# Optimization experiments

Measured on AMD Instinct MI355X. Metric: run time of the kernel, lower is better.

## Reference

```python
import jax, jax.numpy as jnp
import numpy as np

EPS = 1e-5

def conv2d(x, w, stride, pad):
    return jax.lax.conv_general_dilated(
        x, w, window_strides=(stride, stride),
        padding=[(pad, pad), (pad, pad)],
        dimension_numbers=('NCHW', 'OIHW', 'NCHW'))

def batchnorm(x, gamma, beta, mean, var):
    # inference-mode BN over channel dim of NCHW
    inv = jax.lax.rsqrt(var + EPS)
    return (x - mean[None, :, None, None]) * (inv * gamma)[None, :, None, None] + beta[None, :, None, None]

def rational(x, num, den):
    # Rational activation, version A, degrees (5,4):
    #   P(x) = num0 + num1*x + ... + num5*x^5  (Horner)
    #   Q(x) = 1 + sum_{j=1..4} |den_{j-1}| * |x|^j
    p = num[5]
    for i in range(4, -1, -1):
        p = p * x + num[i]
    xa = jnp.abs(x)
    q = jnp.ones_like(x)
    pw = xa
    for j in range(4):
        q = q + jnp.abs(den[j]) * pw
        pw = pw * xa
    return p / q

def multi_variant_rationals(out, num_r, den_r, num_g, den_g, num_b, den_b):
    # channels 0::3 -> r, 1::3 -> g, 2::3 -> b, then re-interleave
    B, C, H, W = out.shape
    o = out.reshape(B, C // 3, 3, H, W)  # channel c = 3*j + k
    r = rational(o[:, :, 0], num_r, den_r)
    g = rational(o[:, :, 1], num_g, den_g)
    b = rational(o[:, :, 2], num_b, den_b)
    return jnp.stack([r, g, b], axis=2).reshape(B, C, H, W)

def setup_inputs() -> dict:
    key = jax.random.key(0)
    ks = jax.random.split(key, 12)
    B, Cin, Cout, H, W = 64, 96, 192, 56, 56
    inp = {
        'x': jax.random.normal(ks[0], (B, Cin, H, W), jnp.float32),
        'w1': jax.random.normal(ks[1], (Cout, Cin, 3, 3), jnp.float32) * 0.05,
        'gamma1': jnp.ones((Cout,), jnp.float32),
        'beta1': jnp.zeros((Cout,), jnp.float32),
        'mean1': jnp.zeros((Cout,), jnp.float32),
        'var1': jnp.ones((Cout,), jnp.float32),
        'num_r': jax.random.normal(ks[2], (6,), jnp.float32) * 0.3,
        'den_r': jax.random.normal(ks[3], (4,), jnp.float32) * 0.3,
        'num_g': jax.random.normal(ks[4], (6,), jnp.float32) * 0.3,
        'den_g': jax.random.normal(ks[5], (4,), jnp.float32) * 0.3,
        'num_b': jax.random.normal(ks[6], (6,), jnp.float32) * 0.3,
        'den_b': jax.random.normal(ks[7], (4,), jnp.float32) * 0.3,
        'w2': jax.random.normal(ks[8], (Cout, Cout, 3, 3), jnp.float32) * 0.05,
        'gamma2': jnp.ones((Cout,), jnp.float32),
        'beta2': jnp.zeros((Cout,), jnp.float32),
        'mean2': jnp.zeros((Cout,), jnp.float32),
        'var2': jnp.ones((Cout,), jnp.float32),
        'ws': jax.random.normal(ks[9], (Cout, Cin, 1, 1), jnp.float32) * 0.05,
        'gammas': jnp.ones((Cout,), jnp.float32),
        'betas': jnp.zeros((Cout,), jnp.float32),
        'means': jnp.zeros((Cout,), jnp.float32),
        'vars_': jnp.ones((Cout,), jnp.float32),
    }
    return inp

def reference(x, w1, gamma1, beta1, mean1, var1,
              num_r, den_r, num_g, den_g, num_b, den_b,
              w2, gamma2, beta2, mean2, var2,
              ws, gammas, betas, means, vars_):
    STRIDE = 2
    out = batchnorm(conv2d(x, w1, STRIDE, 1), gamma1, beta1, mean1, var1)
    out = multi_variant_rationals(out, num_r, den_r, num_g, den_g, num_b, den_b)
    out = batchnorm(conv2d(out, w2, 1, 1), gamma2, beta2, mean2, var2)
    shortcut = batchnorm(conv2d(x, ws, STRIDE, 0), gammas, betas, means, vars_)
    out = out + shortcut
    out = multi_variant_rationals(out, num_r, den_r, num_g, den_g, num_b, den_b)
    return out
```

## Files before the change

kernel.cpp:

```cpp
#include <hip/hip_runtime.h>

#define EPSBN  1e-5f
#define NBLK   392

#define W1B_OFF 0u
#define W2B_OFF 331776u
#define WSB_OFF 995328u
#define CS_OFF  1044480u
#define XT_OFF  1048320u
#define ACT_OFF 39583488u

typedef __attribute__((ext_vector_type(8))) short bf16x8;
typedef __attribute__((ext_vector_type(4))) short bf16x4;
typedef __attribute__((ext_vector_type(4))) float f32x4;

__device__ __forceinline__ short f2bf(float f) {
    unsigned u = __float_as_uint(f);
    u += 0x7fffu + ((u >> 16) & 1u);
    return (short)(u >> 16);
}

__device__ __forceinline__ void gload16(const short* g, short* l) {
    __builtin_amdgcn_global_load_lds(
        (const __attribute__((address_space(1))) void*)g,
        (__attribute__((address_space(3))) void*)l, 16, 0, 0);
}

__device__ __forceinline__ float rational_eval(float v, const float* nm, const float* dn) {
    float p = nm[5];
    p = p * v + nm[4];
    p = p * v + nm[3];
    p = p * v + nm[2];
    p = p * v + nm[1];
    p = p * v + nm[0];
    float xa = fabsf(v);
    float q = 1.0f;
    float pw = xa;
    q += dn[0] * pw; pw *= xa;
    q += dn[1] * pw; pw *= xa;
    q += dn[2] * pw; pw *= xa;
    q += dn[3] * pw;
    float inv = __builtin_amdgcn_rcpf(q);
    inv = inv * (2.0f - q * inv);
    return p * inv;
}

__device__ __forceinline__ void sel_coeffs(int v, const float cnm[3][6], const float cdn[3][4],
                                           float nm[6], float dn[4]) {
#pragma unroll
    for (int i = 0; i < 6; i++) nm[i] = (v == 0) ? cnm[0][i] : ((v == 1) ? cnm[1][i] : cnm[2][i]);
#pragma unroll
    for (int i = 0; i < 4; i++) dn[i] = (v == 0) ? cdn[0][i] : ((v == 1) ? cdn[1][i] : cdn[2][i]);
}

extern "C" __global__ void prep_scales_kernel(
    const float* g1, const float* b1, const float* m1, const float* v1,
    const float* g2, const float* b2, const float* m2, const float* v2,
    const float* gs, const float* bs, const float* ms, const float* vs,
    float* cs)
{
    int i = threadIdx.x;
    if (i < 192) {
        float a1 = g1[i] * rsqrtf(v1[i] + EPSBN);
        float a2 = g2[i] * rsqrtf(v2[i] + EPSBN);
        float a3 = gs[i] * rsqrtf(vs[i] + EPSBN);
        cs[i]       = a1;
        cs[192 + i] = a2;
        cs[384 + i] = a3;
        cs[576 + i] = b1[i] - m1[i] * a1;
        cs[768 + i] = (b2[i] - m2[i] * a2) + (bs[i] - ms[i] * a3);
    }
}

extern "C" __global__ void prep_w_kernel(const float* __restrict__ w, const float* __restrict__ s,
                                         short* __restrict__ wb, int CI_src, int CI_dst, int KP, int total)
{
    int i = blockIdx.x * 256 + threadIdx.x;
    if (i >= total) return;
    int co = i / (CI_dst * KP);
    int r  = i - co * CI_dst * KP;
    int kpos = r / CI_dst;
    int ci = r - kpos * CI_dst;
    wb[i] = (ci < CI_src) ? f2bf(w[(co * CI_src + ci) * KP + kpos] * s[co]) : (short)0;
}

extern "C" __global__ void ring_zero_kernel(short* __restrict__ buf, int H, int C, int total)
{
    int ring = 2 * H + 2 * (H - 2);
    int i = blockIdx.x * 256 + threadIdx.x;
    if (i >= total) return;
    int c = i % C;
    int t = i / C;
    int rp = t % ring;
    int n = t / ring;
    int h, w;
    if (rp < H)           { h = 0;          w = rp; }
    else if (rp < 2 * H)  { h = H - 1;      w = rp - H; }
    else { int k = rp - 2 * H; h = (k >> 1) + 1; w = (k & 1) ? (H - 1) : 0; }
    buf[((n * H + h) * H + w) * C + c] = 0;
}

extern "C" __global__ __launch_bounds__(256)
void xpose_kernel(const float* __restrict__ x, short* __restrict__ xt)
{
    __shared__ float t[96 * 57];
    int b = blockIdx.x;
    int n = b / 56, h = b - n * 56;
    const float* src = x + n * (96 * 3136) + h * 56;
    for (int i = threadIdx.x; i < 96 * 28; i += 256) {
        int c = i / 28, w2 = i - c * 28;
        float2 v = *(const float2*)&src[c * 3136 + w2 * 2];
        t[c * 57 + w2 * 2]     = v.x;
        t[c * 57 + w2 * 2 + 1] = v.y;
    }
    __syncthreads();
    unsigned* dst = (unsigned*)(xt + (n * 56 + h) * 56 * 96);
    for (int i = threadIdx.x; i < 56 * 48; i += 256) {
        int w = i / 96 * 0 + i / 48, cp = i - (i / 48) * 48;
        unsigned lo = (unsigned short)f2bf(t[(2 * cp) * 57 + w]);
        unsigned hi = (unsigned short)f2bf(t[(2 * cp + 1) * 57 + w]);
        dst[w * 48 + cp] = lo | (hi << 16);
    }
}

extern "C" __global__ __launch_bounds__(512, 4)
void convA_kernel(const short* __restrict__ xt,
                  const short* __restrict__ w1b,
                  const short* __restrict__ zbuf,
                  const float* __restrict__ bias1,
                  const float* __restrict__ num_r, const float* __restrict__ den_r,
                  const float* __restrict__ num_g, const float* __restrict__ den_g,
                  const float* __restrict__ num_b, const float* __restrict__ den_b,
                  short* __restrict__ act)
{
    __shared__ short lA[2][192 * 32];
    __shared__ short lB[2][128 * 32];

    const int tid  = threadIdx.x;
    const int lane = tid & 63;
    const int wave = tid >> 6;
    const int wm = wave >> 1, wn = wave & 1;
    const int lbid = (blockIdx.x & 7) * 49 + (blockIdx.x >> 3);
    const int p0   = lbid * 128;

    const int sA = (((tid & 3) ^ ((tid >> 3) & 3))) * 8;
    const int r1 = tid >> 2;
    const int aw1a = r1 * 864 + sA;
    const int aw1b = (128 + r1) * 864 + sA;

    int xb0; bool top, left;
    {
        int p = p0 + r1;
        int n = p / 784; int pr = p - n * 784;
        int oh = pr / 28; int ow = pr - oh * 28;
        xb0 = ((n * 56 + 2 * oh) * 56 + 2 * ow) * 96 + sA;
        top = (oh == 0); left = (ow == 0);
    }

    const int l15 = lane & 15, ksl = lane >> 4;
    int ard[3], brd[4];
#pragma unroll
    for (int m = 0; m < 3; ++m) {
        int row = wm * 48 + m * 16 + l15;
        ard[m] = row * 32 + ((ksl ^ ((row >> 1) & 3)) << 3);
    }
#pragma unroll
    for (int n = 0; n < 4; ++n) {
        int row = wn * 64 + n * 16 + l15;
        brd[n] = row * 32 + ((ksl ^ ((row >> 1) & 3)) << 3);
    }

    auto stage = [&](int buf, int t) {
        int kpos = t / 3, cb = t - 3 * kpos;
        int kh = kpos / 3, kw = kpos - 3 * kh;
        gload16(&w1b[aw1a + t * 32], &lA[buf][wave * 512]);
        if (tid < 256) gload16(&w1b[aw1b + t * 32], &lA[buf][4096 + wave * 512]);
        int bko = ((kh - 1) * 56 + (kw - 1)) * 96 + cb * 32;
        const short* src = (((kh == 0) && top) || ((kw == 0) && left)) ? zbuf : &xt[xb0 + bko];
        gload16(src, &lB[buf][wave * 512]);
    };

    f32x4 acc[3][4];
#pragma unroll
    for (int m = 0; m < 3; m++)
#pragma unroll
        for (int n = 0; n < 4; n++) acc[m][n] = (f32x4){0.f, 0.f, 0.f, 0.f};

    stage(0, 0);
    int cur = 0;
    for (int t = 0; t < 27; ++t) {
        __syncthreads();
        if (t + 1 < 27) stage(cur ^ 1, t + 1);
        bf16x8 af[3];
#pragma unroll
        for (int m = 0; m < 3; ++m) af[m] = *(const bf16x8*)&lA[cur][ard[m]];
#pragma unroll
        for (int n = 0; n < 4; ++n) {
            bf16x8 bv = *(const bf16x8*)&lB[cur][brd[n]];
#pragma unroll
            for (int m = 0; m < 3; ++m)
                acc[m][n] = __builtin_amdgcn_mfma_f32_16x16x32_bf16(af[m], bv, acc[m][n], 0, 0, 0);
        }
        cur ^= 1;
    }

    float cnm[3][6], cdn[3][4];
#pragma unroll
    for (int i = 0; i < 6; i++) { cnm[0][i] = num_r[i]; cnm[1][i] = num_g[i]; cnm[2][i] = num_b[i]; }
#pragma unroll
    for (int i = 0; i < 4; i++) { cdn[0][i] = fabsf(den_r[i]); cdn[1][i] = fabsf(den_g[i]); cdn[2][i] = fabsf(den_b[i]); }

    int abase[4];
#pragma unroll
    for (int n = 0; n < 4; ++n) {
        int pp = p0 + wn * 64 + n * 16 + l15;
        int n2 = pp / 784; int r2 = pp - n2 * 784;
        int oh2 = r2 / 28; int ow2 = r2 - oh2 * 28;
        abase[n] = ((n2 * 30 + oh2 + 1) * 30 + ow2 + 1) * 192;
    }
#pragma unroll
    for (int m = 0; m < 3; ++m) {
        int cob = wm * 48 + m * 16 + (ksl << 2);
        float res[4][4];
#pragma unroll
        for (int r = 0; r < 4; ++r) {
            float nm[6], dn[4];
            sel_coeffs((cob + r) % 3, cnm, cdn, nm, dn);
            float bv = bias1[cob + r];
#pragma unroll
            for (int n = 0; n < 4; ++n)
                res[n][r] = rational_eval(acc[m][n][r] + bv, nm, dn);
        }
#pragma unroll
        for (int n = 0; n < 4; ++n) {
            bf16x4 pk;
#pragma unroll
            for (int r = 0; r < 4; ++r) pk[r] = f2bf(res[n][r]);
            *(bf16x4*)&act[abase[n] + cob] = pk;
        }
    }
}

extern "C" __global__ __launch_bounds__(512, 4)
void convB_kernel(const short* __restrict__ act,
                  const short* __restrict__ xt,
                  const short* __restrict__ w2b,
                  const short* __restrict__ wsb,
                  const float* __restrict__ bias2s,
                  const float* __restrict__ num_r, const float* __restrict__ den_r,
                  const float* __restrict__ num_g, const float* __restrict__ den_g,
                  const float* __restrict__ num_b, const float* __restrict__ den_b,
                  float* __restrict__ outp)
{
    __shared__ short lA[2][192 * 64];
    __shared__ short lB[2][128 * 64];

    const int tid  = threadIdx.x;
    const int lane = tid & 63;
    const int wave = tid >> 6;
    const int wm = wave >> 1, wn = wave & 1;
    const int lbid = (blockIdx.x & 7) * 49 + (blockIdx.x >> 3);
    const int p0   = lbid * 128;

    const int s8 = (((tid & 7) ^ ((tid >> 3) & 7))) * 8;
    const int rA = tid >> 3;

    int awW[3], awS[3];
#pragma unroll
    for (int c = 0; c < 3; ++c) {
        int row = c * 64 + rA;
        awW[c] = row * 1728 + s8;
        awS[c] = row * 128 + s8;
    }
    int abB[2], xcB[2];
#pragma unroll
    for (int c = 0; c < 2; ++c) {
        int p = p0 + c * 64 + rA;
        int n = p / 784; int pr = p - n * 784;
        int oh = pr / 28; int ow = pr - oh * 28;
        abB[c] = ((n * 30 + oh) * 30 + ow) * 192 + s8;
        xcB[c] = ((n * 56 + 2 * oh) * 56 + 2 * ow) * 96 + s8;
    }

    const int l15 = lane & 15, ksl = lane >> 4;
    int ard[2][3], brd[2][4];
#pragma unroll
    for (int kk = 0; kk < 2; ++kk) {
#pragma unroll
        for (int m = 0; m < 3; ++m) {
            int row = wm * 48 + m * 16 + l15;
            ard[kk][m] = row * 64 + ((((kk << 2) | ksl) ^ (row & 7)) << 3);
        }
#pragma unroll
        for (int n = 0; n < 4; ++n) {
            int row = wn * 64 + n * 16 + l15;
            brd[kk][n] = row * 64 + ((((kk << 2) | ksl) ^ (row & 7)) << 3);
        }
    }

    auto stage = [&](int buf, int t) {
        if (t < 2) {
#pragma unroll
            for (int c = 0; c < 3; ++c)
                gload16(&wsb[awS[c] + t * 64], &lA[buf][c * 4096 + wave * 512]);
#pragma unroll
            for (int c = 0; c < 2; ++c)
                gload16(&xt[xcB[c] + t * 64], &lB[buf][c * 4096 + wave * 512]);
        } else {
            int u = t - 2;
            int kpos = u / 3, cb = u - 3 * kpos;
            int kh = kpos / 3, kw = kpos - 3 * kh;
            int bko = (kh * 30 + kw) * 192 + cb * 64;
#pragma unroll
            for (int c = 0; c < 3; ++c)
                gload16(&w2b[awW[c] + u * 64], &lA[buf][c * 4096 + wave * 512]);
#pragma unroll
            for (int c = 0; c < 2; ++c)
                gload16(&act[abB[c] + bko], &lB[buf][c * 4096 + wave * 512]);
        }
    };

    f32x4 acc[3][4];
#pragma unroll
    for (int m = 0; m < 3; m++)
#pragma unroll
        for (int n = 0; n < 4; n++) acc[m][n] = (f32x4){0.f, 0.f, 0.f, 0.f};

    stage(0, 0);
    int cur = 0;
    for (int t = 0; t < 29; ++t) {
        __syncthreads();
        if (t + 1 < 29) stage(cur ^ 1, t + 1);
#pragma unroll
        for (int kk = 0; kk < 2; ++kk) {
            bf16x8 af[3];
#pragma unroll
            for (int m = 0; m < 3; ++m) af[m] = *(const bf16x8*)&lA[cur][ard[kk][m]];
#pragma unroll
            for (int n = 0; n < 4; ++n) {
                bf16x8 bv = *(const bf16x8*)&lB[cur][brd[kk][n]];
#pragma unroll
                for (int m = 0; m < 3; ++m)
                    acc[m][n] = __builtin_amdgcn_mfma_f32_16x16x32_bf16(af[m], bv, acc[m][n], 0, 0, 0);
            }
        }
        cur ^= 1;
    }

    float cnm[3][6], cdn[3][4];
#pragma unroll
    for (int i = 0; i < 6; i++) { cnm[0][i] = num_r[i]; cnm[1][i] = num_g[i]; cnm[2][i] = num_b[i]; }
#pragma unroll
    for (int i = 0; i < 4; i++) { cdn[0][i] = fabsf(den_r[i]); cdn[1][i] = fabsf(den_g[i]); cdn[2][i] = fabsf(den_b[i]); }

    int obase[4];
#pragma unroll
    for (int n = 0; n < 4; ++n) {
        int pp = p0 + wn * 64 + n * 16 + l15;
        int n2 = pp / 784; int r2 = pp - n2 * 784;
        int oh2 = r2 / 28; int ow2 = r2 - oh2 * 28;
        obase[n] = n2 * (192 * 784) + oh2 * 28 + ow2;
    }
#pragma unroll
    for (int m = 0; m < 3; ++m) {
        int cob = wm * 48 + m * 16 + (ksl << 2);
#pragma unroll
        for (int r = 0; r < 4; ++r) {
            float nm[6], dn[4];
            sel_coeffs((cob + r) % 3, cnm, cdn, nm, dn);
            float bv = bias2s[cob + r];
#pragma unroll
            for (int n = 0; n < 4; ++n) {
                int idx = obase[n] + (cob + r) * 784;
                outp[idx] = rational_eval(acc[m][n][r] + bv, nm, dn);
            }
        }
    }
}

extern "C" void kernel_launch(void* const* d_in, const int* in_sizes, int n_in,
                              void* d_out, int out_size, void* d_ws, size_t ws_size,
                              hipStream_t stream)
{
    const float* x      = (const float*)d_in[0];
    const float* w1     = (const float*)d_in[1];
    const float* gamma1 = (const float*)d_in[2];
    const float* beta1  = (const float*)d_in[3];
    const float* mean1  = (const float*)d_in[4];
    const float* var1   = (const float*)d_in[5];
    const float* num_r  = (const float*)d_in[6];
    const float* den_r  = (const float*)d_in[7];
    const float* num_g  = (const float*)d_in[8];
    const float* den_g  = (const float*)d_in[9];
    const float* num_b  = (const float*)d_in[10];
    const float* den_b  = (const float*)d_in[11];
    const float* w2     = (const float*)d_in[12];
    const float* gamma2 = (const float*)d_in[13];
    const float* beta2  = (const float*)d_in[14];
    const float* mean2  = (const float*)d_in[15];
    const float* var2   = (const float*)d_in[16];
    const float* wsc    = (const float*)d_in[17];
    const float* gammas = (const float*)d_in[18];
    const float* betas  = (const float*)d_in[19];
    const float* means  = (const float*)d_in[20];
    const float* vars_  = (const float*)d_in[21];

    char* base = (char*)d_ws;
    short* w1b  = (short*)(base + W1B_OFF);
    short* w2b  = (short*)(base + W2B_OFF);
    short* wsb  = (short*)(base + WSB_OFF);
    float* cs   = (float*)(base + CS_OFF);
    short* xt   = (short*)(base + XT_OFF);
    short* act  = (short*)(base + ACT_OFF);
    float* outp = (float*)d_out;

    float* bias1  = cs + 576;
    float* bias2s = cs + 768;
    const short* zbuf = wsb + 96;

    prep_scales_kernel<<<1, 256, 0, stream>>>(gamma1, beta1, mean1, var1,
                                              gamma2, beta2, mean2, var2,
                                              gammas, betas, means, vars_, cs);

    prep_w_kernel<<<(192 * 96 * 9 + 255) / 256, 256, 0, stream>>>(w1, cs, w1b, 96, 96, 9, 192 * 96 * 9);
    prep_w_kernel<<<(192 * 192 * 9 + 255) / 256, 256, 0, stream>>>(w2, cs + 192, w2b, 192, 192, 9, 192 * 192 * 9);
    prep_w_kernel<<<(192 * 128 + 255) / 256, 256, 0, stream>>>(wsc, cs + 384, wsb, 96, 128, 1, 192 * 128);

    {
        int tot_a = 64 * (2 * 30 + 2 * 28) * 192;
        ring_zero_kernel<<<(tot_a + 255) / 256, 256, 0, stream>>>(act, 30, 192, tot_a);
    }

    xpose_kernel<<<64 * 56, 256, 0, stream>>>(x, xt);

    convA_kernel<<<NBLK, 512, 0, stream>>>(xt, w1b, zbuf, bias1,
                                           num_r, den_r, num_g, den_g, num_b, den_b,
                                           act);

    convB_kernel<<<NBLK, 512, 0, stream>>>(act, xt, w2b, wsb, bias2s,
                                           num_r, den_r, num_g, den_g, num_b, den_b,
                                           outp);
}
```

Baseline: 143.8 us.

## Restructure convB to stage a shared activation patch in LDS and reuse it across taps

convB now assigns each block one image and a band of 7 output rows (196 pixels, 224 including padding). It loads the 9x30x192 activation patch into LDS once with an XOR swizzle, and the 3x3 taps read shifted windows of that patch instead of reloading im2col tiles from global memory for every K step. Only the w2 weights are double-buffered through LDS. The 1x1 shortcut reads its operands straight from global memory into registers. The aim is to cut redundant activation traffic across the 9 taps, at the cost of larger LDS use (occupancy hint drops to 2), padding waste in the N dimension (224 vs 196), and fewer blocks (256).

```diff
diff --git a/kernel.cpp b/kernel.cpp
--- a/kernel.cpp
+++ b/kernel.cpp
@@ -1,7 +1,8 @@
 #include <hip/hip_runtime.h>
 
 #define EPSBN  1e-5f
-#define NBLK   392
+#define NBLK_A 392
+#define NBLK_B 256
 
 #define W1B_OFF 0u
 #define W2B_OFF 331776u
@@ -116,7 +117,7 @@
     __syncthreads();
     unsigned* dst = (unsigned*)(xt + (n * 56 + h) * 56 * 96);
     for (int i = threadIdx.x; i < 56 * 48; i += 256) {
-        int w = i / 96 * 0 + i / 48, cp = i - (i / 48) * 48;
+        int w = i / 48, cp = i - (i / 48) * 48;
         unsigned lo = (unsigned short)f2bf(t[(2 * cp) * 57 + w]);
         unsigned hi = (unsigned short)f2bf(t[(2 * cp + 1) * 57 + w]);
         dst[w * 48 + cp] = lo | (hi << 16);
@@ -241,7 +242,7 @@
     }
 }
 
-extern "C" __global__ __launch_bounds__(512, 4)
+extern "C" __global__ __launch_bounds__(512, 2)
 void convB_kernel(const short* __restrict__ act,
                   const short* __restrict__ xt,
                   const short* __restrict__ w2b,
@@ -252,98 +253,116 @@
                   const float* __restrict__ num_b, const float* __restrict__ den_b,
                   float* __restrict__ outp)
 {
-    __shared__ short lA[2][192 * 64];
-    __shared__ short lB[2][128 * 64];
+    __shared__ short patch[53248];
+    __shared__ short lA[2][6144];
 
     const int tid  = threadIdx.x;
     const int lane = tid & 63;
     const int wave = tid >> 6;
     const int wm = wave >> 1, wn = wave & 1;
-    const int lbid = (blockIdx.x & 7) * 49 + (blockIdx.x >> 3);
-    const int p0   = lbid * 128;
-
-    const int s8 = (((tid & 7) ^ ((tid >> 3) & 7))) * 8;
-    const int rA = tid >> 3;
-
-    int awW[3], awS[3];
-#pragma unroll
-    for (int c = 0; c < 3; ++c) {
-        int row = c * 64 + rA;
-        awW[c] = row * 1728 + s8;
-        awS[c] = row * 128 + s8;
-    }
-    int abB[2], xcB[2];
-#pragma unroll
-    for (int c = 0; c < 2; ++c) {
-        int p = p0 + c * 64 + rA;
-        int n = p / 784; int pr = p - n * 784;
-        int oh = pr / 28; int ow = pr - oh * 28;
-        abB[c] = ((n * 30 + oh) * 30 + ow) * 192 + s8;
-        xcB[c] = ((n * 56 + 2 * oh) * 56 + 2 * ow) * 96 + s8;
-    }
+    const int img = blockIdx.x >> 2;
+    const int oh0 = (blockIdx.x & 3) * 7;
 
     const int l15 = lane & 15, ksl = lane >> 4;
-    int ard[2][3], brd[2][4];
-#pragma unroll
-    for (int kk = 0; kk < 2; ++kk) {
-#pragma unroll
-        for (int m = 0; m < 3; ++m) {
-            int row = wm * 48 + m * 16 + l15;
-            ard[kk][m] = row * 64 + ((((kk << 2) | ksl) ^ (row & 7)) << 3);
-        }
-#pragma unroll
-        for (int n = 0; n < 4; ++n) {
-            int row = wn * 64 + n * 16 + l15;
-            brd[kk][n] = row * 64 + ((((kk << 2) | ksl) ^ (row & 7)) << 3);
-        }
-    }
-
-    auto stage = [&](int buf, int t) {
-        if (t < 2) {
-#pragma unroll
-            for (int c = 0; c < 3; ++c)
-                gload16(&wsb[awS[c] + t * 64], &lA[buf][c * 4096 + wave * 512]);
-#pragma unroll
-            for (int c = 0; c < 2; ++c)
-                gload16(&xt[xcB[c] + t * 64], &lB[buf][c * 4096 + wave * 512]);
-        } else {
-            int u = t - 2;
-            int kpos = u / 3, cb = u - 3 * kpos;
-            int kh = kpos / 3, kw = kpos - 3 * kh;
-            int bko = (kh * 30 + kw) * 192 + cb * 64;
-#pragma unroll
-            for (int c = 0; c < 3; ++c)
-                gload16(&w2b[awW[c] + u * 64], &lA[buf][c * 4096 + wave * 512]);
-#pragma unroll
-            for (int c = 0; c < 2; ++c)
-                gload16(&act[abB[c] + bko], &lB[buf][c * 4096 + wave * 512]);
+
+    int F0[7], F1[7], F2[7], C7[7], SCB[7], OB[7];
+    bool VAL[7];
+#pragma unroll
+    for (int nf = 0; nf < 7; ++nf) {
+        int p = wn * 112 + nf * 16 + l15;
+        int orow = p / 28, ow = p - orow * 28;
+        int r0 = orow;            if (r0 > 8) r0 = 8;
+        int r1_ = orow + 1;       if (r1_ > 8) r1_ = 8;
+        int r2_ = orow + 2;       if (r2_ > 8) r2_ = 8;
+        F0[nf] = r0 * 5760 + ow * 192;
+        F1[nf] = r1_ * 5760 + ow * 192;
+        F2[nf] = r2_ * 5760 + ow * 192;
+        C7[nf] = ow & 7;
+        int ohc = oh0 + orow; if (ohc > 27) ohc = 27;
+        SCB[nf] = ((img * 56 + 2 * ohc) * 56 + 2 * ow) * 96 + ksl * 8;
+        OB[nf]  = img * (192 * 784) + (oh0 + orow) * 28 + ow;
+        VAL[nf] = (p < 196);
+    }
+    int ard[3], scA[3];
+#pragma unroll
+    for (int m = 0; m < 3; ++m) {
+        int row = wm * 48 + m * 16 + l15;
+        ard[m] = row * 32 + ((ksl ^ ((row >> 1) & 3)) << 3);
+        scA[m] = row * 128 + ksl * 8;
+    }
+
+    const int prow0 = (img * 30 + oh0) * 30;
+#pragma unroll
+    for (int j = 0; j < 13; ++j) {
+        int o = (j * 512 + tid) * 8;
+        if (o > 51832) o = 51832;
+        int r = o / 5760;
+        int rem = o - r * 5760;
+        int c = rem / 192;
+        int sl = (rem - c * 192) >> 3;
+        const short* src = &act[(prow0 + r * 30 + c) * 192 + ((sl ^ (c & 7)) << 3)];
+        gload16(src, &patch[(j * 512 + wave * 64) * 8]);
+    }
+
+    f32x4 acc[3][7];
+#pragma unroll
+    for (int m = 0; m < 3; m++)
+#pragma unroll
+        for (int nf = 0; nf < 7; nf++) acc[m][nf] = (f32x4){0.f, 0.f, 0.f, 0.f};
+
+#pragma unroll
+    for (int s = 0; s < 3; ++s) {
+        bf16x8 af[3], bfv[7];
+#pragma unroll
+        for (int m = 0; m < 3; ++m) af[m] = *(const bf16x8*)&wsb[scA[m] + s * 32];
+#pragma unroll
+        for (int nf = 0; nf < 7; ++nf) bfv[nf] = *(const bf16x8*)&xt[SCB[nf] + s * 32];
+#pragma unroll
+        for (int m = 0; m < 3; ++m)
+#pragma unroll
+            for (int nf = 0; nf < 7; ++nf)
+                acc[m][nf] = __builtin_amdgcn_mfma_f32_16x16x32_bf16(af[m], bfv[nf], acc[m][nf], 0, 0, 0);
+    }
+
+    auto stageA = [&](int buf, int u) {
+        int kpos = u / 6, cbk = u - 6 * kpos;
+        int base = kpos * 192 + cbk * 32;
+        {
+            int row = tid >> 2, slot = tid & 3;
+            gload16(&w2b[row * 1728 + base + ((slot ^ ((row >> 1) & 3)) << 3)],
+                    &lA[buf][wave * 512]);
+        }
+        if (tid < 256) {
+            int row = 128 + (tid >> 2), slot = tid & 3;
+            gload16(&w2b[row * 1728 + base + ((slot ^ ((row >> 1) & 3)) << 3)],
+                    &lA[buf][4096 + wave * 512]);
         }
     };
 
-    f32x4 acc[3][4];
-#pragma unroll
-    for (int m = 0; m < 3; m++)
-#pragma unroll
-        for (int n = 0; n < 4; n++) acc[m][n] = (f32x4){0.f, 0.f, 0.f, 0.f};
-
-    stage(0, 0);
+    stageA(0, 0);
+    asm volatile("s_waitcnt vmcnt(0)" ::: "memory");
+    __syncthreads();
+
     int cur = 0;
-    for (int t = 0; t < 29; ++t) {
+    for (int u = 0; u < 54; ++u) {
+        if (u + 1 < 54) stageA(cur ^ 1, u + 1);
+        int kpos = u / 6, cbk = u - 6 * kpos;
+        int kh = kpos / 3, kw = kpos - 3 * kh;
+        int kwo = kw * 192;
+        int sg = cbk * 4 + ksl;
+        bf16x8 af[3];
+#pragma unroll
+        for (int m = 0; m < 3; ++m) af[m] = *(const bf16x8*)&lA[cur][ard[m]];
+#pragma unroll
+        for (int nf = 0; nf < 7; ++nf) {
+            int Fn = (kh == 0) ? F0[nf] : ((kh == 1) ? F1[nf] : F2[nf]);
+            int addr = Fn + kwo + ((sg ^ ((C7[nf] + kw) & 7)) << 3);
+            bf16x8 bv = *(const bf16x8*)&patch[addr];
+#pragma unroll
+            for (int m = 0; m < 3; ++m)
+                acc[m][nf] = __builtin_amdgcn_mfma_f32_16x16x32_bf16(af[m], bv, acc[m][nf], 0, 0, 0);
+        }
         __syncthreads();
-        if (t + 1 < 29) stage(cur ^ 1, t + 1);
-#pragma unroll
-        for (int kk = 0; kk < 2; ++kk) {
-            bf16x8 af[3];
-#pragma unroll
-            for (int m = 0; m < 3; ++m) af[m] = *(const bf16x8*)&lA[cur][ard[kk][m]];
-#pragma unroll
-            for (int n = 0; n < 4; ++n) {
-                bf16x8 bv = *(const bf16x8*)&lB[cur][brd[kk][n]];
-#pragma unroll
-                for (int m = 0; m < 3; ++m)
-                    acc[m][n] = __builtin_amdgcn_mfma_f32_16x16x32_bf16(af[m], bv, acc[m][n], 0, 0, 0);
-            }
-        }
         cur ^= 1;
     }
 
@@ -353,14 +372,6 @@
 #pragma unroll
     for (int i = 0; i < 4; i++) { cdn[0][i] = fabsf(den_r[i]); cdn[1][i] = fabsf(den_g[i]); cdn[2][i] = fabsf(den_b[i]); }
 
-    int obase[4];
-#pragma unroll
-    for (int n = 0; n < 4; ++n) {
-        int pp = p0 + wn * 64 + n * 16 + l15;
-        int n2 = pp / 784; int r2 = pp - n2 * 784;
-        int oh2 = r2 / 28; int ow2 = r2 - oh2 * 28;
-        obase[n] = n2 * (192 * 784) + oh2 * 28 + ow2;
-    }
 #pragma unroll
     for (int m = 0; m < 3; ++m) {
         int cob = wm * 48 + m * 16 + (ksl << 2);
@@ -370,9 +381,9 @@
             sel_coeffs((cob + r) % 3, cnm, cdn, nm, dn);
             float bv = bias2s[cob + r];
 #pragma unroll
-            for (int n = 0; n < 4; ++n) {
-                int idx = obase[n] + (cob + r) * 784;
-                outp[idx] = rational_eval(acc[m][n][r] + bv, nm, dn);
+            for (int nf = 0; nf < 7; ++nf) {
+                if (VAL[nf])
+                    outp[OB[nf] + (cob + r) * 784] = rational_eval(acc[m][nf][r] + bv, nm, dn);
             }
         }
     }
@@ -397,8 +408,8 @@
     const float* w2     = (const float*)d_in[12];
     const float* gamma2 = (const float*)d_in[13];
     const float* beta2  = (const float*)d_in[14];
+    const float* var2   = (const float*)d_in[16];
     const float* mean2  = (const float*)d_in[15];
-    const float* var2   = (const float*)d_in[16];
     const float* wsc    = (const float*)d_in[17];
     const float* gammas = (const float*)d_in[18];
     const float* betas  = (const float*)d_in[19];
@@ -433,11 +444,11 @@
 
     xpose_kernel<<<64 * 56, 256, 0, stream>>>(x, xt);
 
-    convA_kernel<<<NBLK, 512, 0, stream>>>(xt, w1b, zbuf, bias1,
-                                           num_r, den_r, num_g, den_g, num_b, den_b,
-                                           act);
-
-    convB_kernel<<<NBLK, 512, 0, stream>>>(act, xt, w2b, wsb, bias2s,
-                                           num_r, den_r, num_g, den_g, num_b, den_b,
-                                           outp);
-}
+    convA_kernel<<<NBLK_A, 512, 0, stream>>>(xt, w1b, zbuf, bias1,
+                                             num_r, den_r, num_g, den_g, num_b, den_b,
+                                             act);
+
+    convB_kernel<<<NBLK_B, 512, 0, stream>>>(act, xt, w2b, wsb, bias2s,
+                                             num_r, den_r, num_g, den_g, num_b, den_b,
+                                             outp);
+}
```

Measured after the change: 154.4 us. 7.4% more time.
